# Kernel optimization log

Measured on AMD Instinct MI355X. Metric: run time of the kernel, lower is better.

Reference implementation:

```python
import jax, jax.numpy as jnp
import numpy as np

EPS = 1e-6
SKIP_THR = 0.35     # AdaptiveComputeBlock skip_threshold
ENERGY_THR = 0.95   # AdaptiveRankLinear energy_threshold


def rms_norm(x, w):
    return x * jax.lax.rsqrt(jnp.mean(x * x, axis=-1, keepdims=True) + EPS) * w


def ternary_quantize(w):
    # absmean quantization: round(w/scale) clamped to {-1,0,+1}, rescaled
    s = jnp.maximum(jnp.mean(jnp.abs(w)), 1e-8)
    return jnp.clip(jnp.round(w / s), -1.0, 1.0) * s


def setup_inputs() -> dict:
    key = jax.random.key(0)
    ks = jax.random.split(key, 16)
    D, H, depth, R, N = 2048, 8192, 2, 16, 4096
    inp = {
        "x": jax.random.normal(ks[0], (N, D), jnp.float32),
        "acb_norm_w": jnp.ones((depth, D), jnp.float32),
        "router_w": jax.random.normal(ks[1], (depth, D), jnp.float32) * 0.02,
        "w1": jax.random.normal(ks[2], (depth, H, D), jnp.float32) * 0.02,
        "w2": jax.random.normal(ks[3], (depth, D, H), jnp.float32) * 0.02,
        "w3": jax.random.normal(ks[4], (depth, H, D), jnp.float32) * 0.02,
        "acb_gamma": jax.random.uniform(ks[5], (depth, D), jnp.float32) * 1e-2,
        "arl_norm_w": jnp.ones((depth, D), jnp.float32),
        "U": jax.random.normal(ks[6], (depth, D, R), jnp.float32) * 0.02,
        "S": jax.random.normal(ks[7], (depth, R), jnp.float32),
        "V": jax.random.normal(ks[8], (depth, R, D), jnp.float32) * 0.02,
        "arl_gamma": jax.random.uniform(ks[9], (depth, D), jnp.float32) * 1e-2,
        "bit_norm_w": jnp.ones((depth, D), jnp.float32),
        "w_up": jax.random.normal(ks[10], (depth, H, D), jnp.float32) * 0.02,
        "w_down": jax.random.normal(ks[11], (depth, D, H), jnp.float32) * 0.02,
        "bit_gamma": jax.random.uniform(ks[12], (depth, D), jnp.float32) * 1e-2,
    }
    return inp


def reference(x, acb_norm_w, router_w, w1, w2, w3, acb_gamma,
              arl_norm_w, U, S, V, arl_gamma,
              bit_norm_w, w_up, w_down, bit_gamma):
    depth = acb_norm_w.shape[0]
    for d in range(depth):
        # ---- AdaptiveComputeBlock (eval path: hard router mask, no gate scaling)
        xn = rms_norm(x, acb_norm_w[d])                    # [N, D]
        gates = jax.nn.sigmoid(xn @ router_w[d])           # [N]
        active = (gates > SKIP_THR)[..., None]             # [N, 1]
        h = jax.nn.silu(xn @ w1[d].T) * (xn @ w3[d].T)     # [N, H] SwiGLU
        ffn = h @ w2[d].T                                  # [N, D]
        x = x + jnp.where(active, ffn * acb_gamma[d], 0.0)

        # ---- AdaptiveRankLinear (effective-rank mask from singular energy)
        xn = rms_norm(x, arl_norm_w[d])
        s_abs = jnp.abs(S[d])
        cum = jnp.cumsum(s_abs) / jnp.maximum(jnp.sum(s_abs), 1e-8)
        # index i kept iff i < r, r = first index with cum >= threshold (plus 1)
        keep = jnp.concatenate([jnp.ones((1,), bool), cum[:-1] < ENERGY_THR])
        low = (xn @ U[d]) * (S[d] * keep)                  # [N, R]
        x = x + (low @ V[d]) * arl_gamma[d]

        # ---- BitLinear (eval path: ternary weights, fp activations)
        xn = rms_norm(x, bit_norm_w[d])
        hq = jax.nn.silu(xn @ ternary_quantize(w_up[d]).T)  # [N, H]
        x = x + (hq @ ternary_quantize(w_down[d]).T) * bit_gamma[d]
    return x
```

## Files before the change

### kernel.cpp

```cpp
#include <hip/hip_runtime.h>

#define D_DIM 2048
#define H_DIM 8192
#define NTOK  4096
#define R_DIM 16
#define DEPTH 2

typedef float f32x4 __attribute__((ext_vector_type(4)));
typedef __bf16 bf16x8 __attribute__((ext_vector_type(8)));
typedef unsigned short u16x4 __attribute__((ext_vector_type(4)));
typedef unsigned short u16x8 __attribute__((ext_vector_type(8)));
typedef int i32x4 __attribute__((ext_vector_type(4)));
typedef int i32x2 __attribute__((ext_vector_type(2)));

typedef __attribute__((address_space(1))) void void_g;
typedef __attribute__((address_space(3))) void void_l;

__device__ __forceinline__ unsigned short f2bf(float f){
  __bf16 b = (__bf16)f;
  return __builtin_bit_cast(unsigned short, b);
}
__device__ __forceinline__ float bf2f(unsigned short u){
  unsigned int x = ((unsigned int)u) << 16;
  return __builtin_bit_cast(float, x);
}

__device__ __forceinline__ float wredf(float v){
#pragma unroll
  for(int o=32;o;o>>=1) v += __shfl_xor(v,o,64);
  return v;
}
__device__ __forceinline__ float wredmax(float v){
#pragma unroll
  for(int o=32;o;o>>=1) v = fmaxf(v, __shfl_xor(v,o,64));
  return v;
}
__device__ __forceinline__ double wredd(double v){
#pragma unroll
  for(int o=32;o;o>>=1) v += __shfl_xor(v,o,64);
  return v;
}

__device__ __forceinline__ void gload_lds16(const void* g, void* l){
  __builtin_amdgcn_global_load_lds((void_g*)g, (void_l*)l, 16, 0, 0);
}

// ... 261 lines not shown
                                                  signed char* __restrict__ q,
                                                  float* __restrict__ srow)
{
  constexpr int PER = C/256;
  const int row = blockIdx.x, tid = threadIdx.x;
  const int lane = tid & 63, wid = tid >> 6;
  const float* wr = w + (size_t)row*C + tid*PER;
  float v[PER];
  float am = 0.0f;
#pragma unroll
  for(int j=0;j<PER;j+=4){
    f32x4 t = *(const f32x4*)(wr+j);
#pragma unroll
    for(int e=0;e<4;++e){ v[j+e] = t[e]; am = fmaxf(am, fabsf(t[e])); }
  }
  float wm = wredmax(am);
  __shared__ float red[4];
  if(lane==0) red[wid] = wm;
  __syncthreads();
  const float guard = fmaxf(fmaxf(fmaxf(red[0],red[1]),fmaxf(red[2],red[3])),
                            1e-12f);
  const float inv = 127.0f/guard;
  signed char* qr = q + (size_t)row*C + tid*PER;
#pragma unroll
  for(int j=0;j<PER;j+=8){
    i32x2 o;
    o[0] = pack4q(v[j],v[j+1],v[j+2],v[j+3], inv, 127);
    o[1] = pack4q(v[j+4],v[j+5],v[j+6],v[j+7], inv, 127);
    *(i32x2*)(qr+j) = o;
  }
  if(tid==0) srow[row] = guard/127.0f;
}

__global__ __launch_bounds__(256) void abs_part(const float* __restrict__ w,
                                                double* __restrict__ part)
{
  const long long n4 = (long long)H_DIM*D_DIM/4;
  const int tid = threadIdx.x;
  const int lane = tid & 63, wid = tid >> 6;
  float s = 0.0f;
  for(long long i = (long long)blockIdx.x*256 + tid; i < n4;
      i += (long long)gridDim.x*256){
    f32x4 v = ((const f32x4*)w)[i];
    s += fabsf(v[0]) + fabsf(v[1]) + fabsf(v[2]) + fabsf(v[3]);
  }
  double ds = wredd((double)s);
  __shared__ double sred[4];
  if(lane==0) sred[wid] = ds;
  __syncthreads();
  if(tid==0) part[blockIdx.x] = sred[0]+sred[1]+sred[2]+sred[3];
}

__global__ __launch_bounds__(256) void abs_final(const double* __restrict__ part,
                                                 float* __restrict__ scale)
{
  const int tid = threadIdx.x;
  const int lane = tid & 63, wid = tid >> 6;
  double s = 0.0;
  for(int i=tid;i<1024;i+=256) s += part[i];
  s = wredd(s);
  __shared__ double sred[4];
  if(lane==0) sred[wid] = s;
  __syncthreads();
  if(tid==0){
    double m = (sred[0]+sred[1]+sred[2]+sred[3]) / ((double)H_DIM*(double)D_DIM);
    scale[0] = (float)fmax(m, 1e-8);
  }
}

__global__ __launch_bounds__(256) void tquant_i8(const float* __restrict__ w,
                                                 const float* __restrict__ scale,
                                                 signed char* __restrict__ q)
{
  const long long n8 = (long long)H_DIM*D_DIM/8;
  const float inv = 1.0f/scale[0];
  for(long long i = (long long)blockIdx.x*256 + threadIdx.x; i < n8;
      i += (long long)gridDim.x*256){
    f32x4 a = ((const f32x4*)w)[2*i];
    f32x4 b = ((const f32x4*)w)[2*i+1];
    i32x2 o;
    o[0] = pack4q(a[0],a[1],a[2],a[3], inv, 1);
    o[1] = pack4q(b[0],b[1],b[2],b[3], inv, 1);
    ((i32x2*)q)[i] = o;
  }
}

template<int EPI>
__global__ __launch_bounds__(256, 2) void gemmq(
    const signed char* __restrict__ A,
    const signed char* __restrict__ B0,
    const signed char* __restrict__ B1,
    const int Nout, const int K,
    const float* __restrict__ sArow,
    const float* __restrict__ sW0,
    const float* __restrict__ sW1,
    const int* __restrict__ rowmap,
    const int* __restrict__ cntp,
    unsigned short* __restrict__ obf,
    float* __restrict__ xacc,
    const float* __restrict__ gamma)
{
  constexpr bool DUAL    = (EPI==0);
  constexpr bool GATHER  = (EPI==0);
  constexpr bool SCATTER = (EPI==2);
  constexpr bool CMP     = GATHER || SCATTER;

  __shared__ __align__(16) signed char smA[128*128];
  __shared__ __align__(16) signed char smB[128*128];
  __shared__ __align__(16) signed char smB2[DUAL?(128*128):16];

  int cnt = 0;
  if constexpr (CMP) cnt = cntp[0];
  const int padded = CMP ? ((cnt+127)&~127) : (1<<30);

  const int tid  = threadIdx.x;
  const int lane = tid & 63;
  const int wid  = tid >> 6;
  const int wr   = wid >> 1;
  const int wc   = wid & 1;
  const int frow = lane & 15;
  const int k16  = lane >> 4;

  const int nwg = (int)gridDim.x;
  const int bid = (int)blockIdx.x;
  const int swz = ((bid & 7) * (nwg >> 3)) + (bid >> 3);
  const int rowBase = (swz & 31) << 7;
  const int colBase = (swz >> 5) << 7;

  if constexpr (CMP){ if(rowBase >= padded) return; }

  const signed char* Asrc[4];
  const signed char* Bsrc[4];
  const signed char* B2src[4];
#pragma unroll
  for(int u=0;u<4;++u){
    int L = u*256 + tid;
    int row = L >> 3, c = L & 7;
    int soff = (c ^ (row & 7)) * 16;
    int arow;
    if constexpr (GATHER) arow = rowmap[rowBase + row];
    else                  arow = rowBase + row;
    Asrc[u] = A + (size_t)arow*K + soff;
    Bsrc[u] = B0 + (size_t)(colBase + row)*K + soff;
    if constexpr (DUAL) B2src[u] = B1 + (size_t)(colBase + row)*K + soff;
  }

  const i32x4 izero = {0,0,0,0};
  i32x4 acc[4][4];
  i32x4 acc2[4][4];
#pragma unroll
  for(int m=0;m<4;++m)
#pragma unroll
    for(int n=0;n<4;++n){ acc[m][n] = izero; acc2[m][n] = izero; }

  for(int k0=0;k0<K;k0+=128){
#pragma unroll
    for(int u=0;u<4;++u) gload_lds16(Asrc[u]+k0, &smA[u*4096 + tid*16]);
#pragma unroll
    for(int u=0;u<4;++u) gload_lds16(Bsrc[u]+k0, &smB[u*4096 + tid*16]);
    if constexpr (DUAL){
#pragma unroll
      for(int u=0;u<4;++u) gload_lds16(B2src[u]+k0, &smB2[u*4096 + tid*16]);
    }
    __syncthreads();

#pragma unroll
    for(int ks=0;ks<2;++ks){
      i32x4 af[4], bfr[4], bfr2[4];
#pragma unroll
      for(int m=0;m<4;++m){
        int rr = (wr<<6)+(m<<4)+frow;
        int cc = (ks*4 + k16) ^ (rr & 7);
        af[m] = *(const i32x4*)&smA[rr*128 + cc*16];
      }
#pragma unroll
      for(int n=0;n<4;++n){
        int rr = (wc<<6)+(n<<4)+frow;
        int cc = (ks*4 + k16) ^ (rr & 7);
        bfr[n] = *(const i32x4*)&smB[rr*128 + cc*16];
        if constexpr (DUAL) bfr2[n] = *(const i32x4*)&smB2[rr*128 + cc*16];
      }
#pragma unroll
      for(int m=0;m<4;++m)
#pragma unroll
        for(int n=0;n<4;++n){
          acc[m][n] = __builtin_amdgcn_mfma_i32_16x16x64_i8(af[m], bfr[n], acc[m][n], 0,0,0);
          if constexpr (DUAL)
            acc2[m][n] = __builtin_amdgcn_mfma_i32_16x16x64_i8(af[m], bfr2[n], acc2[m][n], 0,0,0);
        }
    }
    __syncthreads();
  }

  float fsW0 = 0.0f;
  if constexpr (EPI==1 || EPI==3) fsW0 = sW0[0];
  const int growB = rowBase + (wr<<6) + (k16<<2);
  const int gcolB = colBase + (wc<<6) + frow;
#pragma unroll
  for(int m=0;m<4;++m){
#pragma unroll
    for(int n=0;n<4;++n){
      const int grow0 = growB + (m<<4);
      const int gcol  = gcolB + (n<<4);
      i32x4 v = acc[m][n];
      if constexpr (EPI==0){
        i32x4 v2 = acc2[m][n];
        const float w0 = sW0[gcol];
        const float w1s = sW1[gcol];
#pragma unroll
        for(int j=0;j<4;++j){
          const int mc = grow0 + j;
          const float sa = sArow[rowmap[mc]];
          float f1 = (float)v[j]  * sa * w0;
          float f3 = (float)v2[j] * sa * w1s;
          float hv = (f1/(1.0f+expf(-f1))) * f3;
          obf[(size_t)mc*Nout + gcol] = f2bf(hv);
        }
      } else if constexpr (EPI==1){
#pragma unroll
        for(int j=0;j<4;++j){
          const float sa = sArow[grow0+j];
          float f = (float)v[j] * sa * fsW0;
          obf[(size_t)(grow0+j)*Nout + gcol] = f2bf(f/(1.0f+expf(-f)));
        }
      } else if constexpr (EPI==2){
        const float gw = sW0[gcol]*gamma[gcol];
#pragma unroll
        for(int j=0;j<4;++j){
          const int mc = grow0 + j;
          if(mc < cnt){
            const float sa = sArow[mc];
            xacc[(size_t)rowmap[mc]*Nout + gcol] += (float)v[j] * sa * gw;
          }
        }
      } else {
        const float gw = fsW0*gamma[gcol];
#pragma unroll
        for(int j=0;j<4;++j){
          const float sa = sArow[grow0+j];
          xacc[(size_t)(grow0+j)*Nout + gcol] += (float)v[j] * sa * gw;
        }
      }
    }
  }
}

__global__ __launch_bounds__(256) void rowpass1(
    const float* __restrict__ x, const float* __restrict__ nw,
    const float* __restrict__ rw, unsigned short* __restrict__ xn,
    float* __restrict__ act)
{
  const int row = blockIdx.x, tid = threadIdx.x;
  const int lane = tid & 63, wid = tid >> 6;
  const float* xr = x + (size_t)row*D_DIM + tid*8;
  f32x4 v0 = *(const f32x4*)xr;
  f32x4 v1 = *(const f32x4*)(xr+4);
  float ssq = 0.0f;
#pragma unroll
  for(int j=0;j<4;++j) ssq += v0[j]*v0[j] + v1[j]*v1[j];
  __shared__ float red[4];
  float t = wredf(ssq);
  if(lane==0) red[wid] = t;
  __syncthreads();
  const float rs = rsqrtf((red[0]+red[1]+red[2]+red[3])*(1.0f/D_DIM) + 1e-6f);
  f32x4 n0 = *(const f32x4*)(nw + tid*8);
  f32x4 n1 = *(const f32x4*)(nw + tid*8 + 4);
  f32x4 r0 = *(const f32x4*)(rw + tid*8);
  f32x4 r1 = *(const f32x4*)(rw + tid*8 + 4);
  float gp = 0.0f;
  u16x4 o0, o1;
#pragma unroll
  for(int j=0;j<4;++j){
    float a = v0[j]*rs*n0[j];
    float b = v1[j]*rs*n1[j];
    gp += a*r0[j] + b*r1[j];
    o0[j] = f2bf(a);
    o1[j] = f2bf(b);
  }
  unsigned short* xp = xn + (size_t)row*D_DIM + tid*8;
  *(u16x4*)xp = o0;
  *(u16x4*)(xp+4) = o1;
  float gd = wredf(gp);
  __syncthreads();
  if(lane==0) red[wid] = gd;
  __syncthreads();
  if(tid==0){
    float dot = red[0]+red[1]+red[2]+red[3];
    float g = 1.0f/(1.0f+expf(-dot));
    act[row] = (g > 0.35f) ? 1.0f : 0.0f;
  }
}

__global__ __launch_bounds__(256) void rowpass2(
    float* __restrict__ x, const float* __restrict__ anw,
    const float* __restrict__ U, const float* __restrict__ Sv,
    const float* __restrict__ V, const float* __restrict__ agam,
    const float* __restrict__ bnw, unsigned short* __restrict__ xn3)
{
  const int row = blockIdx.x, tid = threadIdx.x;
  const int lane = tid & 63, wid = tid >> 6;
  float* xr = x + (size_t)row*D_DIM + tid*8;
  f32x4 v0 = *(const f32x4*)xr;
  f32x4 v1 = *(const f32x4*)(xr+4);
  float ssq = 0.0f;
#pragma unroll
  for(int j=0;j<4;++j) ssq += v0[j]*v0[j] + v1[j]*v1[j];
  __shared__ float red[4];
  float t = wredf(ssq);
  if(lane==0) red[wid] = t;
  __syncthreads();
  const float rs = rsqrtf((red[0]+red[1]+red[2]+red[3])*(1.0f/D_DIM) + 1e-6f);
  f32x4 a0 = *(const f32x4*)(anw + tid*8);
  f32x4 a1 = *(const f32x4*)(anw + tid*8 + 4);
  float xn2[8];
#pragma unroll
  for(int j=0;j<4;++j){ xn2[j] = v0[j]*rs*a0[j]; xn2[4+j] = v1[j]*rs*a1[j]; }
  float pl[16];
#pragma unroll
  for(int r2=0;r2<16;++r2) pl[r2] = 0.0f;
#pragma unroll
  for(int j=0;j<8;++j){
    const int k = tid*8 + j;
    const f32x4* Up = (const f32x4*)(U + (size_t)k*R_DIM);
    f32x4 u0=Up[0], u1=Up[1], u2=Up[2], u3=Up[3];
    const float xv = xn2[j];
#pragma unroll
    for(int q=0;q<4;++q){
      pl[q] += xv*u0[q]; pl[4+q] += xv*u1[q];
      pl[8+q] += xv*u2[q]; pl[12+q] += xv*u3[q];
    }
  }
#pragma unroll
  for(int r2=0;r2<16;++r2) pl[r2] = wredf(pl[r2]);
  __shared__ float lred[4][16];
  if(lane==0){
#pragma unroll
    for(int r2=0;r2<16;++r2) lred[wid][r2] = pl[r2];
  }
  __syncthreads();
  __shared__ float lowS[16];
  if(tid==0){
    float sa[16]; float totS = 0.0f;
#pragma unroll
    for(int r2=0;r2<16;++r2){ sa[r2] = fabsf(Sv[r2]); totS += sa[r2]; }
    totS = fmaxf(totS, 1e-8f);
    float c = 0.0f;
#pragma unroll
    for(int r2=0;r2<16;++r2){
      float lraw = lred[0][r2]+lred[1][r2]+lred[2][r2]+lred[3][r2];
      float keep = (r2==0) ? 1.0f : ((c/totS < 0.95f) ? 1.0f : 0.0f);
      c += sa[r2];
      lowS[r2] = lraw * Sv[r2] * keep;
    }
  }
  __syncthreads();
  f32x4 d0 = {0,0,0,0}, d1 = {0,0,0,0};
#pragma unroll
  for(int r2=0;r2<16;++r2){
    const float lr = lowS[r2];
    const f32x4* Vp = (const f32x4*)(V + (size_t)r2*D_DIM + tid*8);
    f32x4 q0 = Vp[0], q1 = Vp[1];
#pragma unroll
    for(int j=0;j<4;++j){ d0[j] += lr*q0[j]; d1[j] += lr*q1[j]; }
  }
  f32x4 g0 = *(const f32x4*)(agam + tid*8);
  f32x4 g1 = *(const f32x4*)(agam + tid*8 + 4);
  f32x4 xo0, xo1;
  float ssq2 = 0.0f;
#pragma unroll
  for(int j=0;j<4;++j){
    xo0[j] = v0[j] + d0[j]*g0[j];
    xo1[j] = v1[j] + d1[j]*g1[j];
    ssq2 += xo0[j]*xo0[j] + xo1[j]*xo1[j];
  }
  __syncthreads();
  float t2 = wredf(ssq2);
  if(lane==0) red[wid] = t2;
  __syncthreads();
  const float rs2 = rsqrtf((red[0]+red[1]+red[2]+red[3])*(1.0f/D_DIM) + 1e-6f);
  f32x4 b0 = *(const f32x4*)(bnw + tid*8);
  f32x4 b1 = *(const f32x4*)(bnw + tid*8 + 4);
  u16x4 o0, o1;
#pragma unroll
  for(int j=0;j<4;++j){
    o0[j] = f2bf(xo0[j]*rs2*b0[j]);
    o1[j] = f2bf(xo1[j]*rs2*b1[j]);
  }
  *(f32x4*)xr = xo0;
  *(f32x4*)(xr+4) = xo1;
  unsigned short* xp = xn3 + (size_t)row*D_DIM + tid*8;
  *(u16x4*)xp = o0;
  *(u16x4*)(xp+4) = o1;
}

__global__ __launch_bounds__(256) void tquant(const float* __restrict__ w,
                                              const float* __restrict__ scale,
                                              unsigned short* __restrict__ q)
{
  const long long n4 = (long long)H_DIM*D_DIM/4;
  const float s = scale[0];
  for(long long i = (long long)blockIdx.x*256 + threadIdx.x; i < n4;
      i += (long long)gridDim.x*256){
    f32x4 v = ((const f32x4*)w)[i];
    u16x4 o;
#pragma unroll
    for(int j=0;j<4;++j){
      float r = rintf(v[j]/s);
      r = fminf(1.0f, fmaxf(-1.0f, r));
      o[j] = f2bf(r*s);
    }
    ((u16x4*)q)[i] = o;
  }
}

template<int EPI, bool BBF16, bool DUAL>
__global__ __launch_bounds__(256, DUAL?2:3) void gemm128(
    const unsigned short* __restrict__ A,
    const void* __restrict__ B0v,
    const void* __restrict__ B1v,
    const int Nout, const int K,
    unsigned short* __restrict__ obf,
    float* __restrict__ xacc,
    const float* __restrict__ gamma,
    const float* __restrict__ act)
{
  __shared__ __align__(16) unsigned short smA[128*32];
  __shared__ __align__(16) unsigned short smB[128*32];
  __shared__ __align__(16) unsigned short smB2[DUAL?(128*32):8];

  const int tid  = threadIdx.x;
  const int lane = tid & 63;
  const int wid  = tid >> 6;
  const int wr   = wid >> 1;
  const int wc   = wid & 1;
  const int frow = lane & 15;
  const int k16  = lane >> 4;

  const int nwg = (int)gridDim.x;
  const int bid = (int)blockIdx.x;
  const int swz = ((bid & 7) * (nwg >> 3)) + (bid >> 3);
  const int rowBase = (swz & 31) << 7;
  const int colBase = (swz >> 5) << 7;

  int srow[2], schk[2];
#pragma unroll
  for(int r=0;r<2;++r){
    int t = tid + (r<<8);
    srow[r] = t >> 2;
    schk[r] = (t & 3) ^ ((srow[r] >> 1) & 3);
  }

  const f32x4 vzero = {0.0f,0.0f,0.0f,0.0f};
  f32x4 acc[4][4];
  f32x4 acc2[4][4];
#pragma unroll
  for(int m=0;m<4;++m)
#pragma unroll
    for(int n=0;n<4;++n){ acc[m][n] = vzero; acc2[m][n] = vzero; }

  for(int k0=0;k0<K;k0+=32){
#pragma unroll
    for(int r=0;r<2;++r){
      const unsigned short* s = A + (size_t)(rowBase+srow[r])*K + k0 + schk[r]*8;
      gload_lds16(s, &smA[((r<<8)+(wid<<6))*8]);
    }
    if constexpr (BBF16){
      const unsigned short* B0 = (const unsigned short*)B0v;
#pragma unroll
      for(int r=0;r<2;++r){
        const unsigned short* s = B0 + (size_t)(colBase+srow[r])*K + k0 + schk[r]*8;
        gload_lds16(s, &smB[((r<<8)+(wid<<6))*8]);
      }
    } else {
      const float* B0 = (const float*)B0v;
#pragma unroll
      for(int r=0;r<2;++r){
        const float* s = B0 + (size_t)(colBase+srow[r])*K + k0 + schk[r]*8;
        f32x4 f0 = *(const f32x4*)s;
        f32x4 f1 = *(const f32x4*)(s+4);
        u16x8 o;
#pragma unroll
        for(int j=0;j<4;++j){ o[j] = f2bf(f0[j]); o[4+j] = f2bf(f1[j]); }
        *(u16x8*)&smB[(size_t)(tid+(r<<8))*8] = o;
      }
      if constexpr (DUAL){
        const float* B1 = (const float*)B1v;
#pragma unroll
        for(int r=0;r<2;++r){
          const float* s = B1 + (size_t)(colBase+srow[r])*K + k0 + schk[r]*8;
          f32x4 f0 = *(const f32x4*)s;
          f32x4 f1 = *(const f32x4*)(s+4);
          u16x8 o;
#pragma unroll
          for(int j=0;j<4;++j){ o[j] = f2bf(f0[j]); o[4+j] = f2bf(f1[j]); }
          *(u16x8*)&smB2[(size_t)(tid+(r<<8))*8] = o;
        }
      }
    }
    __syncthreads();

    bf16x8 af[4];
#pragma unroll
    for(int m=0;m<4;++m){
      int rr = (wr<<6)+(m<<4)+frow;
      int ch = k16 ^ ((rr>>1)&3);
      af[m] = *(const bf16x8*)&smA[rr*32 + ch*8];
    }
    bf16x8 bfr[4];
    bf16x8 bfr2[4];
#pragma unroll
    for(int n=0;n<4;++n){
      int rr = (wc<<6)+(n<<4)+frow;
      int ch = k16 ^ ((rr>>1)&3);
      bfr[n] = *(const bf16x8*)&smB[rr*32 + ch*8];
      if constexpr (DUAL) bfr2[n] = *(const bf16x8*)&smB2[rr*32 + ch*8];
    }
#pragma unroll
    for(int m=0;m<4;++m)
#pragma unroll
      for(int n=0;n<4;++n){
        acc[m][n] = __builtin_amdgcn_mfma_f32_16x16x32_bf16(af[m], bfr[n], acc[m][n], 0,0,0);
        if constexpr (DUAL)
          acc2[m][n] = __builtin_amdgcn_mfma_f32_16x16x32_bf16(af[m], bfr2[n], acc2[m][n], 0,0,0);
      }
    __syncthreads();
  }

  const int growB = rowBase + (wr<<6) + (k16<<2);
  const int gcolB = colBase + (wc<<6) + frow;
#pragma unroll
  for(int m=0;m<4;++m){
#pragma unroll
    for(int n=0;n<4;++n){
      const int grow0 = growB + (m<<4);
      const int gcol  = gcolB + (n<<4);
      f32x4 v = acc[m][n];
      if constexpr (EPI==0){
        f32x4 v2 = acc2[m][n];
#pragma unroll
        for(int j=0;j<4;++j){
          float t1 = v[j];
          float hv = (t1/(1.0f+expf(-t1))) * v2[j];
          obf[(size_t)(grow0+j)*Nout + gcol] = f2bf(hv);
        }
      } else if constexpr (EPI==1){
#pragma unroll
        for(int j=0;j<4;++j){
          float t1 = v[j];
          obf[(size_t)(grow0+j)*Nout + gcol] = f2bf(t1/(1.0f+expf(-t1)));
        }
      } else if constexpr (EPI==2){
        const float g = gamma[gcol];
#pragma unroll
        for(int j=0;j<4;++j){
          if(act[grow0+j] != 0.0f){
            const size_t ix = (size_t)(grow0+j)*Nout + gcol;
            xacc[ix] += v[j]*g;
          }
        }
      } else {
        const float g = gamma[gcol];
#pragma unroll
        for(int j=0;j<4;++j){
          const size_t ix = (size_t)(grow0+j)*Nout + gcol;
          xacc[ix] += v[j]*g;
        }
      }
    }
  }
}

extern "C" void kernel_launch(void* const* d_in, const int* in_sizes, int n_in,
                              void* d_out, int out_size, void* d_ws, size_t ws_size,
                              hipStream_t stream)
{
  (void)in_sizes; (void)n_in; (void)out_size;
  const float* x_in  = (const float*)d_in[0];
  const float* acbnw = (const float*)d_in[1];
  const float* routw = (const float*)d_in[2];
  const float* w1    = (const float*)d_in[3];
  const float* w2    = (const float*)d_in[4];
  const float* w3    = (const float*)d_in[5];
  const float* acbg  = (const float*)d_in[6];
  const float* arlnw = (const float*)d_in[7];
  const float* U     = (const float*)d_in[8];
  const float* Sv    = (const float*)d_in[9];
  const float* V     = (const float*)d_in[10];
  const float* arlg  = (const float*)d_in[11];
  const float* bitnw = (const float*)d_in[12];
  const float* wup   = (const float*)d_in[13];
  const float* wdn   = (const float*)d_in[14];
  const float* bitg  = (const float*)d_in[15];

  float* xs = (float*)d_out;
  char* ws = (char*)d_ws;

  const bool big = (ws_size >= (size_t)185000000);

  hipMemcpyAsync(xs, x_in, (size_t)NTOK*D_DIM*sizeof(float),
                 hipMemcpyDeviceToDevice, stream);

  if (big) {
    const size_t MB = 1048576;
    unsigned short* hb   = (unsigned short*)(ws);
    signed char*    xnq  = (signed char*)(ws + 64*MB);
    signed char*    hbq  = (signed char*)(ws + 72*MB);
    signed char*    slotA= (signed char*)(ws + 104*MB);
    signed char*    slotB= (signed char*)(ws + 120*MB);
    char* tail = ws + 136*MB;
    float*  sxn   = (float*)(tail);
    float*  sh    = (float*)(tail + 16384);
    float*  act   = (float*)(tail + 32768);
    double* dpart = (double*)(tail + 49152);
    float*  scb   = (float*)(tail + 57344);
    float*  sWA   = (float*)(tail + 65536);
    float*  sWB   = (float*)(tail + 98304);
    int*    rowmap= (int*)(tail + 131072);
    int*    cntp  = (int*)(tail + 147456);

    const int gH = 2048;
    const int gD = 512;

    for(int d=0; d<DEPTH; ++d){
      const size_t oD  = (size_t)d*D_DIM;
      const size_t oHD = (size_t)d*H_DIM*D_DIM;
      const size_t oR  = (size_t)d*R_DIM;
      const size_t oDR = (size_t)d*D_DIM*R_DIM;

      wquant_row<D_DIM><<<H_DIM,256,0,stream>>>(w1+oHD, slotA, sWA);
      wquant_row<D_DIM><<<H_DIM,256,0,stream>>>(w3+oHD, slotB, sWB);
      rowpass1_i8<<<NTOK,256,0,stream>>>(xs, acbnw+oD, routw+oD, xnq, sxn, act);
      buildmap<<<1,256,0,stream>>>(act, rowmap, cntp);
      gemmq<0><<<gH,256,0,stream>>>(
          xnq, slotA, slotB, H_DIM, D_DIM, sxn, sWA, sWB, rowmap, cntp,
          hb, nullptr, nullptr);
      hquant<<<NTOK,256,0,stream>>>(hb, hbq, sh, cntp);
      wquant_row<H_DIM><<<D_DIM,256,0,stream>>>(w2+oHD, slotA, sWA);
      gemmq<2><<<gD,256,0,stream>>>(
          hbq, slotA, nullptr, D_DIM, H_DIM, sh, sWA, nullptr, rowmap, cntp,
          nullptr, xs, acbg+oD);

      rowpass2_i8<<<NTOK,256,0,stream>>>(xs, arlnw+oD, U+oDR, Sv+oR, V+oDR,
                                         arlg+oD, bitnw+oD, xnq, sxn);

      abs_part<<<1024,256,0,stream>>>(wup+oHD, dpart);
      abs_final<<<1,256,0,stream>>>(dpart, scb+0);
      tquant_i8<<<2048,256,0,stream>>>(wup+oHD, scb+0, slotB);
      gemmq<1><<<gH,256,0,stream>>>(
          xnq, slotB, nullptr, H_DIM, D_DIM, sxn, scb+0, nullptr,
          nullptr, nullptr, hb, nullptr, nullptr);
      hquant<<<NTOK,256,0,stream>>>(hb, hbq, sh, nullptr);
      abs_part<<<1024,256,0,stream>>>(wdn+oHD, dpart);
      abs_final<<<1,256,0,stream>>>(dpart, scb+1);
      tquant_i8<<<2048,256,0,stream>>>(wdn+oHD, scb+1, slotA);
      gemmq<3><<<gD,256,0,stream>>>(
          hbq, slotA, nullptr, D_DIM, H_DIM, sh, scb+1, nullptr,
          nullptr, nullptr, nullptr, xs, bitg+oD);
    }
  } else {
    unsigned short* xn = (unsigned short*)(ws);
    unsigned short* hb = (unsigned short*)(ws + 16777216);
    unsigned short* qb = (unsigned short*)(ws + 83886080);
    float*  act   = (float*)(ws + 117440512);
    double* parts = (double*)(ws + 117456896);
    float*  scal  = (float*)(ws + 117465088);

    const int gH = 2048;
    const int gD = 512;

    for(int d=0; d<DEPTH; ++d){
      const size_t oD  = (size_t)d*D_DIM;
      const size_t oHD = (size_t)d*H_DIM*D_DIM;
      const size_t oR  = (size_t)d*R_DIM;
      const size_t oDR = (size_t)d*D_DIM*R_DIM;

      rowpass1<<<NTOK,256,0,stream>>>(xs, acbnw+oD, routw+oD, xn, act);
      gemm128<0,false,true><<<gH,256,0,stream>>>(
          xn, w1+oHD, w3+oHD, H_DIM, D_DIM, hb, nullptr, nullptr, nullptr);
      gemm128<2,false,false><<<gD,256,0,stream>>>(
          hb, w2+oHD, nullptr, D_DIM, H_DIM, nullptr, xs, acbg+oD, act);

      rowpass2<<<NTOK,256,0,stream>>>(xs, arlnw+oD, U+oDR, Sv+oR, V+oDR,
                                      arlg+oD, bitnw+oD, xn);

      abs_part<<<1024,256,0,stream>>>(wup+oHD, parts);
      abs_final<<<1,256,0,stream>>>(parts, scal);
      tquant<<<2048,256,0,stream>>>(wup+oHD, scal, qb);
      gemm128<1,true,false><<<gH,256,0,stream>>>(
          xn, qb, nullptr, H_DIM, D_DIM, hb, nullptr, nullptr, nullptr);

      abs_part<<<1024,256,0,stream>>>(wdn+oHD, parts);
      abs_final<<<1,256,0,stream>>>(parts, scal);
      tquant<<<2048,256,0,stream>>>(wdn+oHD, scal, qb);
      gemm128<3,true,false><<<gD,256,0,stream>>>(
          hb, qb, nullptr, D_DIM, H_DIM, nullptr, xs, bitg+oD, nullptr);
    }
  }
}
```

Baseline: 1.420 ms.

## Switch int8 GEMM to 32x32 MFMA, batch weight quant kernels, drop bf16 path

The int8 GEMM now uses 32x32x32 i8 MFMA tiles with 2x2 accumulators per wave instead of 4x4 16x16x64 tiles. The epilogue switches expf to __expf and is remapped to the 32x32 output layout. Weight quantization is batched: w1/w3 row quant run in one launch, and w_up/w_down abs-mean reduction and ternary quant run as paired launches using a new third slot. The fallback bf16 path for small workspaces is removed, so the code now assumes a larger workspace.

```diff
diff --git a/kernel.cpp b/kernel.cpp
--- a/kernel.cpp
+++ b/kernel.cpp
@@ -7,11 +7,11 @@
 #define DEPTH 2
 
 typedef float f32x4 __attribute__((ext_vector_type(4)));
-typedef __bf16 bf16x8 __attribute__((ext_vector_type(8)));
 typedef unsigned short u16x4 __attribute__((ext_vector_type(4)));
 typedef unsigned short u16x8 __attribute__((ext_vector_type(8)));
+typedef int i32x2 __attribute__((ext_vector_type(2)));
 typedef int i32x4 __attribute__((ext_vector_type(4)));
-typedef int i32x2 __attribute__((ext_vector_type(2)));
+typedef int i32x16 __attribute__((ext_vector_type(16)));
 
 typedef __attribute__((address_space(1))) void void_g;
 typedef __attribute__((address_space(3))) void void_l;
@@ -339,15 +339,48 @@
   if(tid==0) srow[row] = guard/127.0f;
 }
 
-__global__ __launch_bounds__(256) void abs_part(const float* __restrict__ w,
-                                                double* __restrict__ part)
+__global__ __launch_bounds__(256) void wq2(
+    const float* __restrict__ wa, const float* __restrict__ wb,
+    signed char* __restrict__ qa, signed char* __restrict__ qb,
+    float* __restrict__ sa, float* __restrict__ sb)
+{
+  const int bid = blockIdx.x, tid = threadIdx.x;
+  const int lane = tid & 63, wid = tid >> 6;
+  const int row = (bid < H_DIM) ? bid : bid - H_DIM;
+  const float* src = ((bid < H_DIM) ? wa : wb) + (size_t)row*D_DIM + tid*8;
+  signed char* dq  = ((bid < H_DIM) ? qa : qb) + (size_t)row*D_DIM + tid*8;
+  float* sd        = ((bid < H_DIM) ? sa : sb) + row;
+  f32x4 v0 = *(const f32x4*)src;
+  f32x4 v1 = *(const f32x4*)(src+4);
+  float am = 0.0f;
+#pragma unroll
+  for(int e=0;e<4;++e)
+    am = fmaxf(am, fmaxf(fabsf(v0[e]), fabsf(v1[e])));
+  float wm = wredmax(am);
+  __shared__ float red[4];
+  if(lane==0) red[wid] = wm;
+  __syncthreads();
+  const float guard = fmaxf(fmaxf(fmaxf(red[0],red[1]),fmaxf(red[2],red[3])),
+                            1e-12f);
+  const float inv = 127.0f/guard;
+  i32x2 o;
+  o[0] = pack4q(v0[0],v0[1],v0[2],v0[3], inv, 127);
+  o[1] = pack4q(v1[0],v1[1],v1[2],v1[3], inv, 127);
+  *(i32x2*)dq = o;
+  if(tid==0) *sd = guard/127.0f;
+}
+
+__global__ __launch_bounds__(256) void abs_part2(const float* __restrict__ wa,
+                                                 const float* __restrict__ wb,
+                                                 double* __restrict__ part)
 {
   const long long n4 = (long long)H_DIM*D_DIM/4;
-  const int tid = threadIdx.x;
-  const int lane = tid & 63, wid = tid >> 6;
+  const int bid = blockIdx.x, tid = threadIdx.x;
+  const int lane = tid & 63, wid = tid >> 6;
+  const float* w = (bid < 1024) ? wa : wb;
+  const int sub = bid & 1023;
   float s = 0.0f;
-  for(long long i = (long long)blockIdx.x*256 + tid; i < n4;
-      i += (long long)gridDim.x*256){
+  for(long long i = (long long)sub*256 + tid; i < n4; i += 1024*256){
     f32x4 v = ((const f32x4*)w)[i];
     s += fabsf(v[0]) + fabsf(v[1]) + fabsf(v[2]) + fabsf(v[3]);
   }
@@ -355,34 +388,44 @@
   __shared__ double sred[4];
   if(lane==0) sred[wid] = ds;
   __syncthreads();
-  if(tid==0) part[blockIdx.x] = sred[0]+sred[1]+sred[2]+sred[3];
-}
-
-__global__ __launch_bounds__(256) void abs_final(const double* __restrict__ part,
-                                                 float* __restrict__ scale)
+  if(tid==0) part[bid] = sred[0]+sred[1]+sred[2]+sred[3];
+}
+
+__global__ __launch_bounds__(256) void abs_final2(const double* __restrict__ part,
+                                                  float* __restrict__ scale)
 {
   const int tid = threadIdx.x;
   const int lane = tid & 63, wid = tid >> 6;
-  double s = 0.0;
-  for(int i=tid;i<1024;i+=256) s += part[i];
-  s = wredd(s);
-  __shared__ double sred[4];
-  if(lane==0) sred[wid] = s;
+  double s0 = 0.0, s1 = 0.0;
+  for(int i=tid;i<1024;i+=256){ s0 += part[i]; s1 += part[1024+i]; }
+  s0 = wredd(s0); s1 = wredd(s1);
+  __shared__ double sred[2][4];
+  if(lane==0){ sred[0][wid] = s0; sred[1][wid] = s1; }
   __syncthreads();
   if(tid==0){
-    double m = (sred[0]+sred[1]+sred[2]+sred[3]) / ((double)H_DIM*(double)D_DIM);
-    scale[0] = (float)fmax(m, 1e-8);
-  }
-}
-
-__global__ __launch_bounds__(256) void tquant_i8(const float* __restrict__ w,
-                                                 const float* __restrict__ scale,
-                                                 signed char* __restrict__ q)
+    double m0 = (sred[0][0]+sred[0][1]+sred[0][2]+sred[0][3])
+                / ((double)H_DIM*(double)D_DIM);
+    double m1 = (sred[1][0]+sred[1][1]+sred[1][2]+sred[1][3])
+                / ((double)H_DIM*(double)D_DIM);
+    scale[0] = (float)fmax(m0, 1e-8);
+    scale[1] = (float)fmax(m1, 1e-8);
+  }
+}
+
+__global__ __launch_bounds__(256) void tquant2(const float* __restrict__ wa,
+                                               const float* __restrict__ wb,
+                                               const float* __restrict__ scale,
+                                               signed char* __restrict__ qa,
+                                               signed char* __restrict__ qb)
 {
   const long long n8 = (long long)H_DIM*D_DIM/8;
-  const float inv = 1.0f/scale[0];
-  for(long long i = (long long)blockIdx.x*256 + threadIdx.x; i < n8;
-      i += (long long)gridDim.x*256){
+  const int bid = blockIdx.x;
+  const bool first = (bid < 2048);
+  const float* w = first ? wa : wb;
+  signed char* q = first ? qa : qb;
+  const float inv = 1.0f/scale[first ? 0 : 1];
+  const int sub = first ? bid : bid - 2048;
+  for(long long i = (long long)sub*256 + threadIdx.x; i < n8; i += 2048*256){
     f32x4 a = ((const f32x4*)w)[2*i];
     f32x4 b = ((const f32x4*)w)[2*i+1];
     i32x2 o;
@@ -425,8 +468,8 @@
   const int wid  = tid >> 6;
   const int wr   = wid >> 1;
   const int wc   = wid & 1;
-  const int frow = lane & 15;
-  const int k16  = lane >> 4;
+  const int l31  = lane & 31;
+  const int hi   = lane >> 5;
 
   const int nwg = (int)gridDim.x;
   const int bid = (int)blockIdx.x;
@@ -452,13 +495,15 @@
     if constexpr (DUAL) B2src[u] = B1 + (size_t)(colBase + row)*K + soff;
   }
 
-  const i32x4 izero = {0,0,0,0};
-  i32x4 acc[4][4];
-  i32x4 acc2[4][4];
-#pragma unroll
-  for(int m=0;m<4;++m)
-#pragma unroll
-    for(int n=0;n<4;++n){ acc[m][n] = izero; acc2[m][n] = izero; }
+  i32x16 acc[2][2];
+  i32x16 acc2[2][2];
+#pragma unroll
+  for(int m=0;m<2;++m)
+#pragma unroll
+    for(int n=0;n<2;++n){
+#pragma unroll
+      for(int e=0;e<16;++e){ acc[m][n][e] = 0; acc2[m][n][e] = 0; }
+    }
 
   for(int k0=0;k0<K;k0+=128){
 #pragma unroll
@@ -472,28 +517,29 @@
     __syncthreads();
 
 #pragma unroll
-    for(int ks=0;ks<2;++ks){
-      i32x4 af[4], bfr[4], bfr2[4];
-#pragma unroll
-      for(int m=0;m<4;++m){
-        int rr = (wr<<6)+(m<<4)+frow;
-        int cc = (ks*4 + k16) ^ (rr & 7);
+    for(int ks=0;ks<4;++ks){
+      const int c0 = ks*2 + hi;
+      i32x4 af[2], bfr[2], bfr2[2];
+#pragma unroll
+      for(int m=0;m<2;++m){
+        int rr = (wr<<6)+(m<<5)+l31;
+        int cc = c0 ^ (rr & 7);
         af[m] = *(const i32x4*)&smA[rr*128 + cc*16];
       }
 #pragma unroll
-      for(int n=0;n<4;++n){
-        int rr = (wc<<6)+(n<<4)+frow;
-        int cc = (ks*4 + k16) ^ (rr & 7);
+      for(int n=0;n<2;++n){
+        int rr = (wc<<6)+(n<<5)+l31;
+        int cc = c0 ^ (rr & 7);
         bfr[n] = *(const i32x4*)&smB[rr*128 + cc*16];
         if constexpr (DUAL) bfr2[n] = *(const i32x4*)&smB2[rr*128 + cc*16];
       }
 #pragma unroll
-      for(int m=0;m<4;++m)
-#pragma unroll
-        for(int n=0;n<4;++n){
-          acc[m][n] = __builtin_amdgcn_mfma_i32_16x16x64_i8(af[m], bfr[n], acc[m][n], 0,0,0);
+      for(int m=0;m<2;++m)
+#pragma unroll
+        for(int n=0;n<2;++n){
+          acc[m][n] = __builtin_amdgcn_mfma_i32_32x32x32_i8(af[m], bfr[n], acc[m][n], 0,0,0);
           if constexpr (DUAL)
-            acc2[m][n] = __builtin_amdgcn_mfma_i32_16x16x64_i8(af[m], bfr2[n], acc2[m][n], 0,0,0);
+            acc2[m][n] = __builtin_amdgcn_mfma_i32_32x32x32_i8(af[m], bfr2[n], acc2[m][n], 0,0,0);
         }
     }
     __syncthreads();
@@ -501,40 +547,39 @@
 
   float fsW0 = 0.0f;
   if constexpr (EPI==1 || EPI==3) fsW0 = sW0[0];
-  const int growB = rowBase + (wr<<6) + (k16<<2);
-  const int gcolB = colBase + (wc<<6) + frow;
-#pragma unroll
-  for(int m=0;m<4;++m){
-#pragma unroll
-    for(int n=0;n<4;++n){
-      const int grow0 = growB + (m<<4);
-      const int gcol  = gcolB + (n<<4);
-      i32x4 v = acc[m][n];
+#pragma unroll
+  for(int m=0;m<2;++m){
+#pragma unroll
+    for(int n=0;n<2;++n){
+      const int grow0 = rowBase + (wr<<6) + (m<<5) + 4*hi;
+      const int gcol  = colBase + (wc<<6) + (n<<5) + l31;
+      i32x16 v = acc[m][n];
       if constexpr (EPI==0){
-        i32x4 v2 = acc2[m][n];
+        i32x16 v2 = acc2[m][n];
         const float w0 = sW0[gcol];
         const float w1s = sW1[gcol];
 #pragma unroll
-        for(int j=0;j<4;++j){
-          const int mc = grow0 + j;
+        for(int j=0;j<16;++j){
+          const int mc = grow0 + (j&3) + 8*(j>>2);
           const float sa = sArow[rowmap[mc]];
           float f1 = (float)v[j]  * sa * w0;
           float f3 = (float)v2[j] * sa * w1s;
-          float hv = (f1/(1.0f+expf(-f1))) * f3;
+          float hv = (f1/(1.0f+__expf(-f1))) * f3;
           obf[(size_t)mc*Nout + gcol] = f2bf(hv);
         }
       } else if constexpr (EPI==1){
 #pragma unroll
-        for(int j=0;j<4;++j){
-          const float sa = sArow[grow0+j];
+        for(int j=0;j<16;++j){
+          const int mc = grow0 + (j&3) + 8*(j>>2);
+          const float sa = sArow[mc];
           float f = (float)v[j] * sa * fsW0;
-          obf[(size_t)(grow0+j)*Nout + gcol] = f2bf(f/(1.0f+expf(-f)));
+          obf[(size_t)mc*Nout + gcol] = f2bf(f/(1.0f+__expf(-f)));
         }
       } else if constexpr (EPI==2){
         const float gw = sW0[gcol]*gamma[gcol];
 #pragma unroll
-        for(int j=0;j<4;++j){
-          const int mc = grow0 + j;
+        for(int j=0;j<16;++j){
+          const int mc = grow0 + (j&3) + 8*(j>>2);
           if(mc < cnt){
             const float sa = sArow[mc];
             xacc[(size_t)rowmap[mc]*Nout + gcol] += (float)v[j] * sa * gw;
@@ -543,345 +588,21 @@
       } else {
         const float gw = fsW0*gamma[gcol];
 #pragma unroll
-        for(int j=0;j<4;++j){
-          const float sa = sArow[grow0+j];
-          xacc[(size_t)(grow0+j)*Nout + gcol] += (float)v[j] * sa * gw;
+        for(int j=0;j<16;++j){
+          const int mc = grow0 + (j&3) + 8*(j>>2);
+          const float sa = sArow[mc];
+          xacc[(size_t)mc*Nout + gcol] += (float)v[j] * sa * gw;
         }
       }
     }
   }
 }
 
-__global__ __launch_bounds__(256) void rowpass1(
-    const float* __restrict__ x, const float* __restrict__ nw,
-    const float* __restrict__ rw, unsigned short* __restrict__ xn,
-    float* __restrict__ act)
-{
-  const int row = blockIdx.x, tid = threadIdx.x;
-  const int lane = tid & 63, wid = tid >> 6;
-  const float* xr = x + (size_t)row*D_DIM + tid*8;
-  f32x4 v0 = *(const f32x4*)xr;
-  f32x4 v1 = *(const f32x4*)(xr+4);
-  float ssq = 0.0f;
-#pragma unroll
-  for(int j=0;j<4;++j) ssq += v0[j]*v0[j] + v1[j]*v1[j];
-  __shared__ float red[4];
-  float t = wredf(ssq);
-  if(lane==0) red[wid] = t;
-  __syncthreads();
-  const float rs = rsqrtf((red[0]+red[1]+red[2]+red[3])*(1.0f/D_DIM) + 1e-6f);
-  f32x4 n0 = *(const f32x4*)(nw + tid*8);
-  f32x4 n1 = *(const f32x4*)(nw + tid*8 + 4);
-  f32x4 r0 = *(const f32x4*)(rw + tid*8);
-  f32x4 r1 = *(const f32x4*)(rw + tid*8 + 4);
-  float gp = 0.0f;
-  u16x4 o0, o1;
-#pragma unroll
-  for(int j=0;j<4;++j){
-    float a = v0[j]*rs*n0[j];
-    float b = v1[j]*rs*n1[j];
-    gp += a*r0[j] + b*r1[j];
-    o0[j] = f2bf(a);
-    o1[j] = f2bf(b);
-  }
-  unsigned short* xp = xn + (size_t)row*D_DIM + tid*8;
-  *(u16x4*)xp = o0;
-  *(u16x4*)(xp+4) = o1;
-  float gd = wredf(gp);
-  __syncthreads();
-  if(lane==0) red[wid] = gd;
-  __syncthreads();
-  if(tid==0){
-    float dot = red[0]+red[1]+red[2]+red[3];
-    float g = 1.0f/(1.0f+expf(-dot));
-    act[row] = (g > 0.35f) ? 1.0f : 0.0f;
-  }
-}
-
-__global__ __launch_bounds__(256) void rowpass2(
-    float* __restrict__ x, const float* __restrict__ anw,
-    const float* __restrict__ U, const float* __restrict__ Sv,
-    const float* __restrict__ V, const float* __restrict__ agam,
-    const float* __restrict__ bnw, unsigned short* __restrict__ xn3)
-{
-  const int row = blockIdx.x, tid = threadIdx.x;
-  const int lane = tid & 63, wid = tid >> 6;
-  float* xr = x + (size_t)row*D_DIM + tid*8;
-  f32x4 v0 = *(const f32x4*)xr;
-  f32x4 v1 = *(const f32x4*)(xr+4);
-  float ssq = 0.0f;
-#pragma unroll
-  for(int j=0;j<4;++j) ssq += v0[j]*v0[j] + v1[j]*v1[j];
-  __shared__ float red[4];
-  float t = wredf(ssq);
-  if(lane==0) red[wid] = t;
-  __syncthreads();
-  const float rs = rsqrtf((red[0]+red[1]+red[2]+red[3])*(1.0f/D_DIM) + 1e-6f);
-  f32x4 a0 = *(const f32x4*)(anw + tid*8);
-  f32x4 a1 = *(const f32x4*)(anw + tid*8 + 4);
-  float xn2[8];
-#pragma unroll
-  for(int j=0;j<4;++j){ xn2[j] = v0[j]*rs*a0[j]; xn2[4+j] = v1[j]*rs*a1[j]; }
-  float pl[16];
-#pragma unroll
-  for(int r2=0;r2<16;++r2) pl[r2] = 0.0f;
-#pragma unroll
-  for(int j=0;j<8;++j){
-    const int k = tid*8 + j;
-    const f32x4* Up = (const f32x4*)(U + (size_t)k*R_DIM);
-    f32x4 u0=Up[0], u1=Up[1], u2=Up[2], u3=Up[3];
-    const float xv = xn2[j];
-#pragma unroll
-    for(int q=0;q<4;++q){
-      pl[q] += xv*u0[q]; pl[4+q] += xv*u1[q];
-      pl[8+q] += xv*u2[q]; pl[12+q] += xv*u3[q];
-    }
-  }
-#pragma unroll
-  for(int r2=0;r2<16;++r2) pl[r2] = wredf(pl[r2]);
-  __shared__ float lred[4][16];
-  if(lane==0){
-#pragma unroll
-    for(int r2=0;r2<16;++r2) lred[wid][r2] = pl[r2];
-  }
-  __syncthreads();
-  __shared__ float lowS[16];
-  if(tid==0){
-    float sa[16]; float totS = 0.0f;
-#pragma unroll
-    for(int r2=0;r2<16;++r2){ sa[r2] = fabsf(Sv[r2]); totS += sa[r2]; }
-    totS = fmaxf(totS, 1e-8f);
-    float c = 0.0f;
-#pragma unroll
-    for(int r2=0;r2<16;++r2){
-      float lraw = lred[0][r2]+lred[1][r2]+lred[2][r2]+lred[3][r2];
-      float keep = (r2==0) ? 1.0f : ((c/totS < 0.95f) ? 1.0f : 0.0f);
-      c += sa[r2];
-      lowS[r2] = lraw * Sv[r2] * keep;
-    }
-  }
-  __syncthreads();
-  f32x4 d0 = {0,0,0,0}, d1 = {0,0,0,0};
-#pragma unroll
-  for(int r2=0;r2<16;++r2){
-    const float lr = lowS[r2];
-    const f32x4* Vp = (const f32x4*)(V + (size_t)r2*D_DIM + tid*8);
-    f32x4 q0 = Vp[0], q1 = Vp[1];
-#pragma unroll
-    for(int j=0;j<4;++j){ d0[j] += lr*q0[j]; d1[j] += lr*q1[j]; }
-  }
-  f32x4 g0 = *(const f32x4*)(agam + tid*8);
-  f32x4 g1 = *(const f32x4*)(agam + tid*8 + 4);
-  f32x4 xo0, xo1;
-  float ssq2 = 0.0f;
-#pragma unroll
-  for(int j=0;j<4;++j){
-    xo0[j] = v0[j] + d0[j]*g0[j];
-    xo1[j] = v1[j] + d1[j]*g1[j];
-    ssq2 += xo0[j]*xo0[j] + xo1[j]*xo1[j];
-  }
-  __syncthreads();
-  float t2 = wredf(ssq2);
-  if(lane==0) red[wid] = t2;
-  __syncthreads();
-  const float rs2 = rsqrtf((red[0]+red[1]+red[2]+red[3])*(1.0f/D_DIM) + 1e-6f);
-  f32x4 b0 = *(const f32x4*)(bnw + tid*8);
-  f32x4 b1 = *(const f32x4*)(bnw + tid*8 + 4);
-  u16x4 o0, o1;
-#pragma unroll
-  for(int j=0;j<4;++j){
-    o0[j] = f2bf(xo0[j]*rs2*b0[j]);
-    o1[j] = f2bf(xo1[j]*rs2*b1[j]);
-  }
-  *(f32x4*)xr = xo0;
-  *(f32x4*)(xr+4) = xo1;
-  unsigned short* xp = xn3 + (size_t)row*D_DIM + tid*8;
-  *(u16x4*)xp = o0;
-  *(u16x4*)(xp+4) = o1;
-}
-
-__global__ __launch_bounds__(256) void tquant(const float* __restrict__ w,
-                                              const float* __restrict__ scale,
-                                              unsigned short* __restrict__ q)
-{
-  const long long n4 = (long long)H_DIM*D_DIM/4;
-  const float s = scale[0];
-  for(long long i = (long long)blockIdx.x*256 + threadIdx.x; i < n4;
-      i += (long long)gridDim.x*256){
-    f32x4 v = ((const f32x4*)w)[i];
-    u16x4 o;
-#pragma unroll
-    for(int j=0;j<4;++j){
-      float r = rintf(v[j]/s);
-      r = fminf(1.0f, fmaxf(-1.0f, r));
-      o[j] = f2bf(r*s);
-    }
-    ((u16x4*)q)[i] = o;
-  }
-}
-
-template<int EPI, bool BBF16, bool DUAL>
-__global__ __launch_bounds__(256, DUAL?2:3) void gemm128(
-    const unsigned short* __restrict__ A,
-    const void* __restrict__ B0v,
-    const void* __restrict__ B1v,
-    const int Nout, const int K,
-    unsigned short* __restrict__ obf,
-    float* __restrict__ xacc,
-    const float* __restrict__ gamma,
-    const float* __restrict__ act)
-{
-  __shared__ __align__(16) unsigned short smA[128*32];
-  __shared__ __align__(16) unsigned short smB[128*32];
-  __shared__ __align__(16) unsigned short smB2[DUAL?(128*32):8];
-
-  const int tid  = threadIdx.x;
-  const int lane = tid & 63;
-  const int wid  = tid >> 6;
-  const int wr   = wid >> 1;
-  const int wc   = wid & 1;
-  const int frow = lane & 15;
-  const int k16  = lane >> 4;
-
-  const int nwg = (int)gridDim.x;
-  const int bid = (int)blockIdx.x;
-  const int swz = ((bid & 7) * (nwg >> 3)) + (bid >> 3);
-  const int rowBase = (swz & 31) << 7;
-  const int colBase = (swz >> 5) << 7;
-
-  int srow[2], schk[2];
-#pragma unroll
-  for(int r=0;r<2;++r){
-    int t = tid + (r<<8);
-    srow[r] = t >> 2;
-    schk[r] = (t & 3) ^ ((srow[r] >> 1) & 3);
-  }
-
-  const f32x4 vzero = {0.0f,0.0f,0.0f,0.0f};
-  f32x4 acc[4][4];
-  f32x4 acc2[4][4];
-#pragma unroll
-  for(int m=0;m<4;++m)
-#pragma unroll
-    for(int n=0;n<4;++n){ acc[m][n] = vzero; acc2[m][n] = vzero; }
-
-  for(int k0=0;k0<K;k0+=32){
-#pragma unroll
-    for(int r=0;r<2;++r){
-      const unsigned short* s = A + (size_t)(rowBase+srow[r])*K + k0 + schk[r]*8;
-      gload_lds16(s, &smA[((r<<8)+(wid<<6))*8]);
-    }
-    if constexpr (BBF16){
-      const unsigned short* B0 = (const unsigned short*)B0v;
-#pragma unroll
-      for(int r=0;r<2;++r){
-        const unsigned short* s = B0 + (size_t)(colBase+srow[r])*K + k0 + schk[r]*8;
-        gload_lds16(s, &smB[((r<<8)+(wid<<6))*8]);
-      }
-    } else {
-      const float* B0 = (const float*)B0v;
-#pragma unroll
-      for(int r=0;r<2;++r){
-        const float* s = B0 + (size_t)(colBase+srow[r])*K + k0 + schk[r]*8;
-        f32x4 f0 = *(const f32x4*)s;
-        f32x4 f1 = *(const f32x4*)(s+4);
-        u16x8 o;
-#pragma unroll
-        for(int j=0;j<4;++j){ o[j] = f2bf(f0[j]); o[4+j] = f2bf(f1[j]); }
-        *(u16x8*)&smB[(size_t)(tid+(r<<8))*8] = o;
-      }
-      if constexpr (DUAL){
-        const float* B1 = (const float*)B1v;
-#pragma unroll
-        for(int r=0;r<2;++r){
-          const float* s = B1 + (size_t)(colBase+srow[r])*K + k0 + schk[r]*8;
-          f32x4 f0 = *(const f32x4*)s;
-          f32x4 f1 = *(const f32x4*)(s+4);
-          u16x8 o;
-#pragma unroll
-          for(int j=0;j<4;++j){ o[j] = f2bf(f0[j]); o[4+j] = f2bf(f1[j]); }
-          *(u16x8*)&smB2[(size_t)(tid+(r<<8))*8] = o;
-        }
-      }
-    }
-    __syncthreads();
-
-    bf16x8 af[4];
-#pragma unroll
-    for(int m=0;m<4;++m){
-      int rr = (wr<<6)+(m<<4)+frow;
-      int ch = k16 ^ ((rr>>1)&3);
-      af[m] = *(const bf16x8*)&smA[rr*32 + ch*8];
-    }
-    bf16x8 bfr[4];
-    bf16x8 bfr2[4];
-#pragma unroll
-    for(int n=0;n<4;++n){
-      int rr = (wc<<6)+(n<<4)+frow;
-      int ch = k16 ^ ((rr>>1)&3);
-      bfr[n] = *(const bf16x8*)&smB[rr*32 + ch*8];
-      if constexpr (DUAL) bfr2[n] = *(const bf16x8*)&smB2[rr*32 + ch*8];
-    }
-#pragma unroll
-    for(int m=0;m<4;++m)
-#pragma unroll
-      for(int n=0;n<4;++n){
-        acc[m][n] = __builtin_amdgcn_mfma_f32_16x16x32_bf16(af[m], bfr[n], acc[m][n], 0,0,0);
-        if constexpr (DUAL)
-          acc2[m][n] = __builtin_amdgcn_mfma_f32_16x16x32_bf16(af[m], bfr2[n], acc2[m][n], 0,0,0);
-      }
-    __syncthreads();
-  }
-
-  const int growB = rowBase + (wr<<6) + (k16<<2);
-  const int gcolB = colBase + (wc<<6) + frow;
-#pragma unroll
-  for(int m=0;m<4;++m){
-#pragma unroll
-    for(int n=0;n<4;++n){
-      const int grow0 = growB + (m<<4);
-      const int gcol  = gcolB + (n<<4);
-      f32x4 v = acc[m][n];
-      if constexpr (EPI==0){
-        f32x4 v2 = acc2[m][n];
-#pragma unroll
-        for(int j=0;j<4;++j){
-          float t1 = v[j];
-          float hv = (t1/(1.0f+expf(-t1))) * v2[j];
-          obf[(size_t)(grow0+j)*Nout + gcol] = f2bf(hv);
-        }
-      } else if constexpr (EPI==1){
-#pragma unroll
-        for(int j=0;j<4;++j){
-          float t1 = v[j];
-          obf[(size_t)(grow0+j)*Nout + gcol] = f2bf(t1/(1.0f+expf(-t1)));
-        }
-      } else if constexpr (EPI==2){
-        const float g = gamma[gcol];
-#pragma unroll
-        for(int j=0;j<4;++j){
-          if(act[grow0+j] != 0.0f){
-            const size_t ix = (size_t)(grow0+j)*Nout + gcol;
-            xacc[ix] += v[j]*g;
-          }
-        }
-      } else {
-        const float g = gamma[gcol];
-#pragma unroll
-        for(int j=0;j<4;++j){
-          const size_t ix = (size_t)(grow0+j)*Nout + gcol;
-          xacc[ix] += v[j]*g;
-        }
-      }
-    }
-  }
-}
-
 extern "C" void kernel_launch(void* const* d_in, const int* in_sizes, int n_in,
                               void* d_out, int out_size, void* d_ws, size_t ws_size,
                               hipStream_t stream)
 {
-  (void)in_sizes; (void)n_in; (void)out_size;
+  (void)in_sizes; (void)n_in; (void)out_size; (void)ws_size;
   const float* x_in  = (const float*)d_in[0];
   const float* acbnw = (const float*)d_in[1];
   const float* routw = (const float*)d_in[2];
@@ -902,105 +623,60 @@
   float* xs = (float*)d_out;
   char* ws = (char*)d_ws;
 
-  const bool big = (ws_size >= (size_t)185000000);
-
   hipMemcpyAsync(xs, x_in, (size_t)NTOK*D_DIM*sizeof(float),
                  hipMemcpyDeviceToDevice, stream);
 
-  if (big) {
-    const size_t MB = 1048576;
-    unsigned short* hb   = (unsigned short*)(ws);
-    signed char*    xnq  = (signed char*)(ws + 64*MB);
-    signed char*    hbq  = (signed char*)(ws + 72*MB);
-    signed char*    slotA= (signed char*)(ws + 104*MB);
-    signed char*    slotB= (signed char*)(ws + 120*MB);
-    char* tail = ws + 136*MB;
-    float*  sxn   = (float*)(tail);
-    float*  sh    = (float*)(tail + 16384);
-    float*  act   = (float*)(tail + 32768);
-    double* dpart = (double*)(tail + 49152);
-    float*  scb   = (float*)(tail + 57344);
-    float*  sWA   = (float*)(tail + 65536);
-    float*  sWB   = (float*)(tail + 98304);
-    int*    rowmap= (int*)(tail + 131072);
-    int*    cntp  = (int*)(tail + 147456);
-
-    const int gH = 2048;
-    const int gD = 512;
-
-    for(int d=0; d<DEPTH; ++d){
-      const size_t oD  = (size_t)d*D_DIM;
-      const size_t oHD = (size_t)d*H_DIM*D_DIM;
-      const size_t oR  = (size_t)d*R_DIM;
-      const size_t oDR = (size_t)d*D_DIM*R_DIM;
-
-      wquant_row<D_DIM><<<H_DIM,256,0,stream>>>(w1+oHD, slotA, sWA);
-      wquant_row<D_DIM><<<H_DIM,256,0,stream>>>(w3+oHD, slotB, sWB);
-      rowpass1_i8<<<NTOK,256,0,stream>>>(xs, acbnw+oD, routw+oD, xnq, sxn, act);
-      buildmap<<<1,256,0,stream>>>(act, rowmap, cntp);
-      gemmq<0><<<gH,256,0,stream>>>(
-          xnq, slotA, slotB, H_DIM, D_DIM, sxn, sWA, sWB, rowmap, cntp,
-          hb, nullptr, nullptr);
-      hquant<<<NTOK,256,0,stream>>>(hb, hbq, sh, cntp);
-      wquant_row<H_DIM><<<D_DIM,256,0,stream>>>(w2+oHD, slotA, sWA);
-      gemmq<2><<<gD,256,0,stream>>>(
-          hbq, slotA, nullptr, D_DIM, H_DIM, sh, sWA, nullptr, rowmap, cntp,
-          nullptr, xs, acbg+oD);
-
-      rowpass2_i8<<<NTOK,256,0,stream>>>(xs, arlnw+oD, U+oDR, Sv+oR, V+oDR,
-                                         arlg+oD, bitnw+oD, xnq, sxn);
-
-      abs_part<<<1024,256,0,stream>>>(wup+oHD, dpart);
-      abs_final<<<1,256,0,stream>>>(dpart, scb+0);
-      tquant_i8<<<2048,256,0,stream>>>(wup+oHD, scb+0, slotB);
-      gemmq<1><<<gH,256,0,stream>>>(
-          xnq, slotB, nullptr, H_DIM, D_DIM, sxn, scb+0, nullptr,
-          nullptr, nullptr, hb, nullptr, nullptr);
-      hquant<<<NTOK,256,0,stream>>>(hb, hbq, sh, nullptr);
-      abs_part<<<1024,256,0,stream>>>(wdn+oHD, dpart);
-      abs_final<<<1,256,0,stream>>>(dpart, scb+1);
-      tquant_i8<<<2048,256,0,stream>>>(wdn+oHD, scb+1, slotA);
-      gemmq<3><<<gD,256,0,stream>>>(
-          hbq, slotA, nullptr, D_DIM, H_DIM, sh, scb+1, nullptr,
-          nullptr, nullptr, nullptr, xs, bitg+oD);
-    }
-  } else {
-    unsigned short* xn = (unsigned short*)(ws);
-    unsigned short* hb = (unsigned short*)(ws + 16777216);
-    unsigned short* qb = (unsigned short*)(ws + 83886080);
-    float*  act   = (float*)(ws + 117440512);
-    double* parts = (double*)(ws + 117456896);
-    float*  scal  = (float*)(ws + 117465088);
-
-    const int gH = 2048;
-    const int gD = 512;
-
-    for(int d=0; d<DEPTH; ++d){
-      const size_t oD  = (size_t)d*D_DIM;
-      const size_t oHD = (size_t)d*H_DIM*D_DIM;
-      const size_t oR  = (size_t)d*R_DIM;
-      const size_t oDR = (size_t)d*D_DIM*R_DIM;
-
-      rowpass1<<<NTOK,256,0,stream>>>(xs, acbnw+oD, routw+oD, xn, act);
-      gemm128<0,false,true><<<gH,256,0,stream>>>(
-          xn, w1+oHD, w3+oHD, H_DIM, D_DIM, hb, nullptr, nullptr, nullptr);
-      gemm128<2,false,false><<<gD,256,0,stream>>>(
-          hb, w2+oHD, nullptr, D_DIM, H_DIM, nullptr, xs, acbg+oD, act);
-
-      rowpass2<<<NTOK,256,0,stream>>>(xs, arlnw+oD, U+oDR, Sv+oR, V+oDR,
-                                      arlg+oD, bitnw+oD, xn);
-
-      abs_part<<<1024,256,0,stream>>>(wup+oHD, parts);
-      abs_final<<<1,256,0,stream>>>(parts, scal);
-      tquant<<<2048,256,0,stream>>>(wup+oHD, scal, qb);
-      gemm128<1,true,false><<<gH,256,0,stream>>>(
-          xn, qb, nullptr, H_DIM, D_DIM, hb, nullptr, nullptr, nullptr);
-
-      abs_part<<<1024,256,0,stream>>>(wdn+oHD, parts);
-      abs_final<<<1,256,0,stream>>>(parts, scal);
-      tquant<<<2048,256,0,stream>>>(wdn+oHD, scal, qb);
-      gemm128<3,true,false><<<gD,256,0,stream>>>(
-          hb, qb, nullptr, D_DIM, H_DIM, nullptr, xs, bitg+oD, nullptr);
-    }
-  }
-}
+  const size_t MB = 1048576;
+  unsigned short* hb   = (unsigned short*)(ws);
+  signed char*    xnq  = (signed char*)(ws + 64*MB);
+  signed char*    hbq  = (signed char*)(ws + 72*MB);
+  signed char*    slotA= (signed char*)(ws + 104*MB);
+  signed char*    slotB= (signed char*)(ws + 120*MB);
+  signed char*    slotC= (signed char*)(ws + 136*MB);
+  char* tail = ws + 152*MB;
+  float*  sxn   = (float*)(tail);
+  float*  sh    = (float*)(tail + 16384);
+  float*  act   = (float*)(tail + 32768);
+  double* dpart = (double*)(tail + 49152);
+  float*  scb   = (float*)(tail + 65536);
+  float*  sWA   = (float*)(tail + 69632);
+  float*  sWB   = (float*)(tail + 102400);
+  int*    rowmap= (int*)(tail + 135168);
+  int*    cntp  = (int*)(tail + 151552);
+
+  const int gH = 2048;
+  const int gD = 512;
+
+  for(int d=0; d<DEPTH; ++d){
+    const size_t oD  = (size_t)d*D_DIM;
+    const size_t oHD = (size_t)d*H_DIM*D_DIM;
+    const size_t oR  = (size_t)d*R_DIM;
+    const size_t oDR = (size_t)d*D_DIM*R_DIM;
+
+    wq2<<<2*H_DIM,256,0,stream>>>(w1+oHD, w3+oHD, slotA, slotB, sWA, sWB);
+    rowpass1_i8<<<NTOK,256,0,stream>>>(xs, acbnw+oD, routw+oD, xnq, sxn, act);
+    buildmap<<<1,256,0,stream>>>(act, rowmap, cntp);
+    gemmq<0><<<gH,256,0,stream>>>(
+        xnq, slotA, slotB, H_DIM, D_DIM, sxn, sWA, sWB, rowmap, cntp,
+        hb, nullptr, nullptr);
+    hquant<<<NTOK,256,0,stream>>>(hb, hbq, sh, cntp);
+    wquant_row<H_DIM><<<D_DIM,256,0,stream>>>(w2+oHD, slotA, sWA);
+    gemmq<2><<<gD,256,0,stream>>>(
+        hbq, slotA, nullptr, D_DIM, H_DIM, sh, sWA, nullptr, rowmap, cntp,
+        nullptr, xs, acbg+oD);
+
+    rowpass2_i8<<<NTOK,256,0,stream>>>(xs, arlnw+oD, U+oDR, Sv+oR, V+oDR,
+                                       arlg+oD, bitnw+oD, xnq, sxn);
+
+    abs_part2<<<2048,256,0,stream>>>(wup+oHD, wdn+oHD, dpart);
+    abs_final2<<<1,256,0,stream>>>(dpart, scb);
+    tquant2<<<4096,256,0,stream>>>(wup+oHD, wdn+oHD, scb, slotB, slotC);
+    gemmq<1><<<gH,256,0,stream>>>(
+        xnq, slotB, nullptr, H_DIM, D_DIM, sxn, scb+0, nullptr,
+        nullptr, nullptr, hb, nullptr, nullptr);
+    hquant<<<NTOK,256,0,stream>>>(hb, hbq, sh, nullptr);
+    gemmq<3><<<gD,256,0,stream>>>(
+        hbq, slotC, nullptr, D_DIM, H_DIM, sh, scb+1, nullptr,
+        nullptr, nullptr, nullptr, xs, bitg+oD);
+  }
+}
```

New measurement: 1.466 ms. 1.03x slower.
